# Optimization experiments

Measured on AMD Instinct MI355X. Metric: run time of the kernel, lower is better.

## Reference

```python
import jax, jax.numpy as jnp
import numpy as np
from math import sqrt

IN_DIM = 4096
OUT_DIM = 32
TW = 2            # tree_width (forced to 2 by the forward's pairwise stacking)
TREE_DEPTH = 22
T = TREE_DEPTH - 1  # number of loop iterations (module decrements tree_depth)


def _w(k, out_dim, in_dim):
    # mimics init_weights_unif: U(-1,1)/sqrt(out_dim) + eye (preserve=True default)
    x = (jax.random.uniform(k, (out_dim, in_dim)) * 2 - 1) / sqrt(out_dim)
    return x + jnp.eye(out_dim, in_dim)


def _b(k, dim):
    return (jax.random.uniform(k, (dim,)) * 2 - 1) / sqrt(dim)


def setup_inputs() -> dict:
    key = jax.random.key(0)
    ks = jax.random.split(key, 14)
    return {
        "x": jax.random.normal(ks[0], (IN_DIM,), dtype=jnp.float32),
        "in_left_layer": _w(ks[1], TW, IN_DIM),
        "in_right_layer": _w(ks[2], TW, IN_DIM),
        "in_left_bias": _b(ks[3], TW),
        "in_right_bias": _b(ks[4], TW),
        "tree_left_layers": jnp.stack([_w(k, TW, TW) for k in jax.random.split(ks[5], T)]),
        "tree_right_layers": jnp.stack([_w(k, TW, TW) for k in jax.random.split(ks[6], T)]),
        "tree_left_biases": jnp.stack([_b(k, TW) for k in jax.random.split(ks[7], T)]),
        "tree_right_biases": jnp.stack([_b(k, TW) for k in jax.random.split(ks[8], T)]),
        "out_layer0": _w(ks[9], OUT_DIM, IN_DIM),
        "out_layers": jnp.stack([_w(k, OUT_DIM, TW) for k in jax.random.split(ks[10], T)]),
        "out_bias": _b(ks[11], OUT_DIM),
    }


def reference(x, in_left_layer, in_right_layer, in_left_bias, in_right_bias,
              tree_left_layers, tree_right_layers, tree_left_biases,
              tree_right_biases, out_layer0, out_layers, out_bias):
    # Faithful to BinTreeNetwork.forward: the per-j torch.tensor([li_j, ri_j])
    # construction is exactly jnp.stack([left, right], axis=1); the
    # ComponentNetwork is constructed in __init__ but never used in forward.
    left = x @ in_left_layer.T + in_left_bias      # (TW,)
    right = x @ in_right_layer.T + in_right_bias   # (TW,)
    out = x @ out_layer0.T                          # (OUT_DIM,)
    n_iter = tree_left_layers.shape[0]
    for i in range(n_iter):  # fixed small structural loop; shapes differ per level
        # res: binary-tree expansion, shape (2,)*(i+2); res[j,0]=left[j], res[j,1]=right[j]
        res = jnp.stack([left, right], axis=1)
        left = res @ tree_left_layers[i].T + tree_left_biases[i]
        right = res @ tree_right_layers[i].T + tree_right_biases[i]
        # out broadcasts: (2,)*i+(OUT_DIM,) + (2,)*(i+1)+(OUT_DIM,)
        out = out + res @ out_layers[i].T
    return out + out_bias  # shape (2,)*T + (OUT_DIM,)
```

## Files before the change

kernel.cpp:

```cpp
#include <hip/hip_runtime.h>
#include <hip/hip_bf16.h>


#define P0 (1u << 19)
#define C14OFF (1u << 20)
#define C16OFF (1u << 21)

typedef float floatx4 __attribute__((ext_vector_type(4)));

__global__ __launch_bounds__(1024) void k_dots(
    const float* __restrict__ x,
    const float* __restrict__ inL,
    const float* __restrict__ inR,
    const float* __restrict__ outL0,
    float* __restrict__ ws)
{
    __shared__ float red[16];
    const int d = blockIdx.x;
    const int tid = threadIdx.x;
    const float* row =
        (d < 2) ? inL + d * 4096 :
        (d < 4) ? inR + (d - 2) * 4096 :
                  outL0 + (d - 4) * 4096;
    floatx4 a = ((const floatx4*)row)[tid];
    floatx4 b = ((const floatx4*)x)[tid];
    float s = a.x * b.x + a.y * b.y + a.z * b.z + a.w * b.w;
    #pragma unroll
    for (int off = 32; off; off >>= 1) s += __shfl_down(s, off, 64);
    if ((tid & 63) == 0) red[tid >> 6] = s;
    __syncthreads();
    if (tid < 16) {
        float v = red[tid];
        #pragma unroll
        for (int off = 8; off; off >>= 1) v += __shfl_down(v, off, 16);
        if (tid == 0) ws[P0 + 1664 + d] = v;
    }
}

__global__ __launch_bounds__(1024) void k_levels(
    const float* __restrict__ inLb,
    const float* __restrict__ inRb,
    const float* __restrict__ treeL,
    const float* __restrict__ treeR,
    const float* __restrict__ treeLb,
    const float* __restrict__ treeRb,
    const float* __restrict__ outLs,
    const float* __restrict__ outB,
    float* __restrict__ ws)
{
    const int tid = threadIdx.x;
    float* base  = ws + P0;
    float* outLf = ws + P0 + 32;
    float* tLf   = ws + P0 + 1376;
    float* tRf   = ws + P0 + 1460;
    float* tLbf  = ws + P0 + 1544;
    float* tRbf  = ws + P0 + 1586;
    const float* dots = ws + P0 + 1664;
    float* C7    = ws + P0 + 2048;

    for (int i = tid; i < 21 * 64; i += 1024) outLf[i] = outLs[i];
    if (tid < 84)                      tLf[tid]        = treeL[tid];
    else if (tid < 168)                tRf[tid - 84]   = treeR[tid - 84];
    else if (tid < 210)                tLbf[tid - 168] = treeLb[tid - 168];
    else if (tid < 252)                tRbf[tid - 210] = treeRb[tid - 210];
    if (tid < 32) base[tid] = dots[4 + tid] + outB[tid];
    if (tid < 2) {
        ws[tid * 2 + 0] = dots[tid]     + inLb[tid];
        ws[tid * 2 + 1] = dots[2 + tid] + inRb[tid];
    }
    __syncthreads();

    for (int i = 1; i <= 13; ++i) {
        const float* prev = ws + ((1u << (i + 1)) - 4);
        float* cur        = ws + ((1u << (i + 2)) - 4);
        const int rows = 1 << (i + 1);
        const int lowmask = (1 << (i - 1)) - 1;
        for (int m = tid; m < rows; m += 1024) {
            const int src = ((m >> i) << (i - 1)) | (m & lowmask);
            const int s = (m >> (i - 1)) & 1;
            const float* W  = (s ? tRf  : tLf)  + (i - 1) * 4;
            const float* bb = (s ? tRbf : tLbf) + (i - 1) * 2;
            const float p0 = prev[src * 2], p1 = prev[src * 2 + 1];
            cur[m * 2 + 0] = W[0] * p0 + W[1] * p1 + bb[0];
            cur[m * 2 + 1] = W[2] * p0 + W[3] * p1 + bb[1];
        }
        __syncthreads();
    }

    for (int idx = tid; idx < 8192; idx += 1024) {
        const int m = idx >> 5, o = idx & 31;
        float s = base[o];
        #pragma unroll
        for (int i = 0; i < 8; ++i) {
            const float* ri = ws + ((1u << (i + 2)) - 4) + (m & ((2 << i) - 1)) * 2;
            s += ri[0] * outLf[i * 64 + o * 2] + ri[1] * outLf[i * 64 + o * 2 + 1];
        }
        C7[idx] = s;
    }
}

__global__ __launch_bounds__(256) void k_mid(float* __restrict__ ws)
{
    const int blk = blockIdx.x;
    int j, b;
    if      (blk < 16) { j = 14; b = blk; }
    else if (blk < 48) { j = 15; b = blk - 16; }
    else               { j = 16; b = blk - 48; }

    const float* tLf  = ws + P0 + 1376;
    const float* tRf  = ws + P0 + 1460;
    const float* tLbf = ws + P0 + 1544;
    const float* tRbf = ws + P0 + 1586;

    unsigned m = (unsigned)b << 11;
    const unsigned basej = m;
    unsigned sbits = 0;
    for (int l = j; l > 13; --l) {
        sbits |= ((m >> (l - 1)) & 1u) << l;
        m = ((m >> l) << (l - 1)) | (m & ((1u << (l - 1)) - 1));
    }

    const int r0 = threadIdx.x * 8;
    const floatx4* s4 = (const floatx4*)(ws + ((1u << 15) - 4) + (m + r0) * 2);
    floatx4 a0 = s4[0], a1 = s4[1], a2 = s4[2], a3 = s4[3];
    float r[8][2] = {{a0.x,a0.y},{a0.z,a0.w},{a1.x,a1.y},{a1.z,a1.w},
                     {a2.x,a2.y},{a2.z,a2.w},{a3.x,a3.y},{a3.z,a3.w}};

    for (int l = 14; l <= j; ++l) {
        const int s = (sbits >> l) & 1;
        const float* W  = (s ? tRf  : tLf)  + (l - 1) * 4;
        const float* bb = (s ? tRbf : tLbf) + (l - 1) * 2;
        const float w00 = W[0], w01 = W[1], w10 = W[2], w11 = W[3];
        const float b0 = bb[0], b1 = bb[1];
        #pragma unroll
        for (int q = 0; q < 8; ++q) {
            const float p0 = r[q][0], p1 = r[q][1];
            r[q][0] = w00 * p0 + w01 * p1 + b0;
            r[q][1] = w10 * p0 + w11 * p1 + b1;
        }
    }

    floatx4* d4 = (floatx4*)(ws + ((1u << (j + 2)) - 4) + (basej + r0) * 2);
    d4[0] = (floatx4){r[0][0], r[0][1], r[1][0], r[1][1]};
    d4[1] = (floatx4){r[2][0], r[2][1], r[3][0], r[3][1]};
    d4[2] = (floatx4){r[4][0], r[4][1], r[5][0], r[5][1]};
    d4[3] = (floatx4){r[6][0], r[6][1], r[7][0], r[7][1]};
}

__global__ __launch_bounds__(256) void k_c16(float* __restrict__ ws)
{
    const unsigned m = blockIdx.x * 256u + threadIdx.x;
    const float* outLf = ws + P0 + 32;
    const float* C7    = ws + P0 + 2048;

    float acc[32];
    const floatx4* c4 = (const floatx4*)(C7 + (m & 255u) * 32);
    #pragma unroll
    for (int q = 0; q < 8; ++q) {
        floatx4 v = c4[q];
        acc[q * 4 + 0] = v.x; acc[q * 4 + 1] = v.y;
        acc[q * 4 + 2] = v.z; acc[q * 4 + 3] = v.w;
    }
    #pragma unroll
    for (int i = 8; i <= 16; ++i) {
        const float2 v = *(const float2*)(ws + ((1u << (i + 2)) - 4)
                                             + (m & ((2u << i) - 1)) * 2);
        const float* cf = outLf + i * 64;
        #pragma unroll
        for (int o = 0; o < 32; ++o)
            acc[o] += v.x * cf[o * 2] + v.y * cf[o * 2 + 1];
    }
    floatx4* dst = (floatx4*)(ws + C16OFF + (size_t)m * 32);
    #pragma unroll
    for (int q = 0; q < 8; ++q)
        dst[q] = (floatx4){acc[q * 4 + 0], acc[q * 4 + 1],
                           acc[q * 4 + 2], acc[q * 4 + 3]};
}

__global__ __launch_bounds__(256) void k_c14(float* __restrict__ ws)
{
    const unsigned m = blockIdx.x * 256u + threadIdx.x;
    const float* outLf = ws + P0 + 32;
    const float* C7    = ws + P0 + 2048;

    float acc[32];
    const floatx4* c4 = (const floatx4*)(C7 + (m & 255u) * 32);
    #pragma unroll
    for (int q = 0; q < 8; ++q) {
        floatx4 v = c4[q];
        acc[q * 4 + 0] = v.x; acc[q * 4 + 1] = v.y;
        acc[q * 4 + 2] = v.z; acc[q * 4 + 3] = v.w;
    }
    #pragma unroll
    for (int i = 8; i <= 14; ++i) {
        const float2 v = *(const float2*)(ws + ((1u << (i + 2)) - 4)
                                             + (m & ((2u << i) - 1)) * 2);
        const float* cf = outLf + i * 64;
        #pragma unroll
        for (int o = 0; o < 32; ++o)
            acc[o] += v.x * cf[o * 2] + v.y * cf[o * 2 + 1];
    }
    floatx4* dst = (floatx4*)(ws + C14OFF + m * 32);
    #pragma unroll
    for (int q = 0; q < 8; ++q)
        dst[q] = (floatx4){acc[q * 4 + 0], acc[q * 4 + 1],
                           acc[q * 4 + 2], acc[q * 4 + 3]};
}

__global__ __launch_bounds__(256) void k_final_c16(const float* __restrict__ ws,
                                                   float* __restrict__ out)
{
    __shared__ floatx4 st[256 * 8];
    const int tid = threadIdx.x;
    const unsigned B = blockIdx.x * 256u + tid;
    const float* outLf = ws + P0 + 32;
    const float* tLf   = ws + P0 + 1376;
    const float* tRf   = ws + P0 + 1460;
    const float* tLbf  = ws + P0 + 1544;
    const float* tRbf  = ws + P0 + 1586;
    const float* C16   = ws + C16OFF;

    float acc[32];
    {
        const floatx4* c4 = (const floatx4*)(C16 + (size_t)(B & 0x1FFFFu) * 32);
        #pragma unroll
        for (int q = 0; q < 8; ++q) {
            floatx4 v = c4[q];
            acc[q * 4 + 0] = v.x; acc[q * 4 + 1] = v.y;
            acc[q * 4 + 2] = v.z; acc[q * 4 + 3] = v.w;
        }
    }

    {
        const unsigned Blo = B & 0xFFFFu;
        const float* r16 = ws + ((1u << 18) - 4);
        float2 vA = *(const float2*)(r16 + Blo * 2);
        float2 vC = *(const float2*)(r16 + (Blo + 65536u) * 2);
        float A0 = vA.x, A1 = vA.y;
        float c0 = vC.x, c1 = vC.y;
        #pragma unroll
        for (int l = 17; l <= 20; ++l) {
            const int s = (B >> (l - 1)) & 1;
            const float* WL = tLf + (l - 1) * 4;
            const float* WR = tRf + (l - 1) * 4;
            const float* bL = tLbf + (l - 1) * 2;
            const float* bR = tRbf + (l - 1) * 2;
            const float w00 = s ? WR[0] : WL[0], w01 = s ? WR[1] : WL[1];
            const float w10 = s ? WR[2] : WL[2], w11 = s ? WR[3] : WL[3];
            const float b0  = s ? bR[0] : bL[0], b1  = s ? bR[1] : bL[1];
            const float nA0 = w00 * A0 + w01 * A1 + b0;
            const float nA1 = w10 * A0 + w11 * A1 + b1;
            const float nc0 = w00 * c0 + w01 * c1 + b0;
            const float nc1 = w10 * c0 + w11 * c1 + b1;
            A0 = nA0; A1 = nA1; c0 = nc0; c1 = nc1;
            const int pick = (B >> l) & 1;
            const float q0 = pick ? c0 : A0, q1 = pick ? c1 : A1;
            const float* cf = outLf + l * 64;
            #pragma unroll
            for (int o = 0; o < 32; ++o)
                acc[o] += q0 * cf[o * 2] + q1 * cf[o * 2 + 1];
        }
    }

    #pragma unroll
    for (int q = 0; q < 8; ++q) {
        st[tid * 8 + (q ^ (tid & 7))] =
            (floatx4){acc[q * 4 + 0], acc[q * 4 + 1],
                      acc[q * 4 + 2], acc[q * 4 + 3]};
    }
    __syncthreads();
    {
        const int w = tid >> 6, lane = tid & 63;
        const int x = (lane & 7) ^ (lane >> 3);
        floatx4* dst = (floatx4*)(out + (size_t)blockIdx.x * 8192u
                                      + (unsigned)w * 2048u + (unsigned)lane * 4u);
        #pragma unroll
        for (int j = 0; j < 8; ++j) {
            const int m = w * 64 + j * 8 + (lane >> 3);
            __builtin_nontemporal_store(st[m * 8 + x], dst + j * 64);
        }
    }
}

__global__ __launch_bounds__(256) void k_final_fold(const float* __restrict__ ws,
                                                    float* __restrict__ out)
{
    __shared__ floatx4 st[256 * 8];
    const int tid = threadIdx.x;
    const unsigned B = blockIdx.x * 256u + tid;
    const float* outLf = ws + P0 + 32;
    const float* tLf   = ws + P0 + 1376;
    const float* tRf   = ws + P0 + 1460;
    const float* tLbf  = ws + P0 + 1544;
    const float* tRbf  = ws + P0 + 1586;
    const float* C14   = ws + C14OFF;

    float acc[32];
    {
        const floatx4* c4 = (const floatx4*)(C14 + (B & 0x7FFFu) * 32);
        #pragma unroll
        for (int q = 0; q < 8; ++q) {
            floatx4 v = c4[q];
            acc[q * 4 + 0] = v.x; acc[q * 4 + 1] = v.y;
            acc[q * 4 + 2] = v.z; acc[q * 4 + 3] = v.w;
        }
    }
    {
        const float2 v = *(const float2*)(ws + ((1u << 17) - 4)
                                             + (B & 0xFFFFu) * 2);
        const float* cf = outLf + 15 * 64;
        #pragma unroll
        for (int o = 0; o < 32; ++o)
            acc[o] += v.x * cf[o * 2] + v.y * cf[o * 2 + 1];
    }
    {
        const unsigned Blo = B & 0xFFFFu;
        const float* r16 = ws + ((1u << 18) - 4);
        float2 vA = *(const float2*)(r16 + Blo * 2);
        float2 vC = *(const float2*)(r16 + (Blo + 65536u) * 2);
        float A0 = vA.x, A1 = vA.y;
        float c0 = vC.x, c1 = vC.y;
        {
            const int pick = (B >> 16) & 1;
            const float q0 = pick ? c0 : A0, q1 = pick ? c1 : A1;
            const float* cf = outLf + 16 * 64;
            #pragma unroll
            for (int o = 0; o < 32; ++o)
                acc[o] += q0 * cf[o * 2] + q1 * cf[o * 2 + 1];
        }
        #pragma unroll
        for (int l = 17; l <= 20; ++l) {
            const int s = (B >> (l - 1)) & 1;
            const float* WL = tLf + (l - 1) * 4;
            const float* WR = tRf + (l - 1) * 4;
            const float* bL = tLbf + (l - 1) * 2;
            const float* bR = tRbf + (l - 1) * 2;
            const float w00 = s ? WR[0] : WL[0], w01 = s ? WR[1] : WL[1];
            const float w10 = s ? WR[2] : WL[2], w11 = s ? WR[3] : WL[3];
            const float b0  = s ? bR[0] : bL[0], b1  = s ? bR[1] : bL[1];
            const float nA0 = w00 * A0 + w01 * A1 + b0;
            const float nA1 = w10 * A0 + w11 * A1 + b1;
            const float nc0 = w00 * c0 + w01 * c1 + b0;
            const float nc1 = w10 * c0 + w11 * c1 + b1;
            A0 = nA0; A1 = nA1; c0 = nc0; c1 = nc1;
            const int pick = (B >> l) & 1;
            const float q0 = pick ? c0 : A0, q1 = pick ? c1 : A1;
            const float* cf = outLf + l * 64;
            #pragma unroll
            for (int o = 0; o < 32; ++o)
                acc[o] += q0 * cf[o * 2] + q1 * cf[o * 2 + 1];
        }
    }
    #pragma unroll
    for (int q = 0; q < 8; ++q) {
        st[tid * 8 + (q ^ (tid & 7))] =
            (floatx4){acc[q * 4 + 0], acc[q * 4 + 1],
                      acc[q * 4 + 2], acc[q * 4 + 3]};
    }
    __syncthreads();
    {
        const int w = tid >> 6, lane = tid & 63;
        const int x = (lane & 7) ^ (lane >> 3);
        floatx4* dst = (floatx4*)(out + (size_t)blockIdx.x * 8192u
                                      + (unsigned)w * 2048u + (unsigned)lane * 4u);
        #pragma unroll
        for (int j = 0; j < 8; ++j) {
            const int m = w * 64 + j * 8 + (lane >> 3);
            __builtin_nontemporal_store(st[m * 8 + x], dst + j * 64);
        }
    }
}

__global__ __launch_bounds__(256) void k_final_legacy(const float* __restrict__ ws,
                                                      float* __restrict__ out)
{
    __shared__ floatx4 st[256 * 8];
    const int tid = threadIdx.x;
    const unsigned B = blockIdx.x * 256u + tid;
    const float* outLf = ws + P0 + 32;
    const float* tLf   = ws + P0 + 1376;
    const float* tRf   = ws + P0 + 1460;
    const float* tLbf  = ws + P0 + 1544;
    const float* tRbf  = ws + P0 + 1586;
    const float* C7    = ws + P0 + 2048;

    float acc[32];
    {
        const floatx4* c4 = (const floatx4*)(C7 + (B & 255u) * 32);
        #pragma unroll
        for (int q = 0; q < 8; ++q) {
            floatx4 v = c4[q];
            acc[q * 4 + 0] = v.x; acc[q * 4 + 1] = v.y;
            acc[q * 4 + 2] = v.z; acc[q * 4 + 3] = v.w;
        }
    }
    float p[8][2];
    #pragma unroll
    for (int i = 8; i <= 15; ++i) {
        const float2* ri = (const float2*)(ws + ((1u << (i + 2)) - 4)
                                              + (B & ((2u << i) - 1)) * 2);
        float2 v = *ri;
        p[i - 8][0] = v.x;
        p[i - 8][1] = v.y;
    }
    #pragma unroll
    for (int i = 0; i < 8; ++i) {
        const float* cf = outLf + (i + 8) * 64;
        const float q0 = p[i][0], q1 = p[i][1];
        #pragma unroll
        for (int o = 0; o < 32; ++o)
            acc[o] += q0 * cf[o * 2] + q1 * cf[o * 2 + 1];
    }
    {
        const unsigned Blo = B & 0xFFFFu;
        const float* r16 = ws + ((1u << 18) - 4);
        float2 vA = *(const float2*)(r16 + Blo * 2);
        float2 vC = *(const float2*)(r16 + (Blo + 65536u) * 2);
        float A0 = vA.x, A1 = vA.y;
        float c0 = vC.x, c1 = vC.y;
        {
            const int pick = (B >> 16) & 1;
            const float q0 = pick ? c0 : A0, q1 = pick ? c1 : A1;
            const float* cf = outLf + 16 * 64;
            #pragma unroll
            for (int o = 0; o < 32; ++o)
                acc[o] += q0 * cf[o * 2] + q1 * cf[o * 2 + 1];
        }
        #pragma unroll
        for (int l = 17; l <= 20; ++l) {
            const int s = (B >> (l - 1)) & 1;
            const float* WL = tLf + (l - 1) * 4;
            const float* WR = tRf + (l - 1) * 4;
            const float* bL = tLbf + (l - 1) * 2;
            const float* bR = tRbf + (l - 1) * 2;
            const float w00 = s ? WR[0] : WL[0], w01 = s ? WR[1] : WL[1];
            const float w10 = s ? WR[2] : WL[2], w11 = s ? WR[3] : WL[3];
            const float b0  = s ? bR[0] : bL[0], b1  = s ? bR[1] : bL[1];
            const float nA0 = w00 * A0 + w01 * A1 + b0;
            const float nA1 = w10 * A0 + w11 * A1 + b1;
            const float nc0 = w00 * c0 + w01 * c1 + b0;
            const float nc1 = w10 * c0 + w11 * c1 + b1;
            A0 = nA0; A1 = nA1; c0 = nc0; c1 = nc1;
            const int pick = (B >> l) & 1;
            const float q0 = pick ? c0 : A0, q1 = pick ? c1 : A1;
            const float* cf = outLf + l * 64;
            #pragma unroll
            for (int o = 0; o < 32; ++o)
                acc[o] += q0 * cf[o * 2] + q1 * cf[o * 2 + 1];
        }
    }
    #pragma unroll
    for (int q = 0; q < 8; ++q) {
        st[tid * 8 + (q ^ (tid & 7))] =
            (floatx4){acc[q * 4 + 0], acc[q * 4 + 1],
                      acc[q * 4 + 2], acc[q * 4 + 3]};
    }
    __syncthreads();
    {
        const int w = tid >> 6, lane = tid & 63;
        const int x = (lane & 7) ^ (lane >> 3);
        floatx4* dst = (floatx4*)(out + (size_t)blockIdx.x * 8192u
                                      + (unsigned)w * 2048u + (unsigned)lane * 4u);
        #pragma unroll
        for (int j = 0; j < 8; ++j) {
            const int m = w * 64 + j * 8 + (lane >> 3);
            __builtin_nontemporal_store(st[m * 8 + x], dst + j * 64);
        }
    }
}

extern "C" void kernel_launch(void* const* d_in, const int* in_sizes, int n_in,
                              void* d_out, int out_size, void* d_ws, size_t ws_size,
                              hipStream_t stream) {
    const float* x     = (const float*)d_in[0];
    const float* inL   = (const float*)d_in[1];
    const float* inR   = (const float*)d_in[2];
    const float* inLb  = (const float*)d_in[3];
    const float* inRb  = (const float*)d_in[4];
    const float* treeL = (const float*)d_in[5];
    const float* treeR = (const float*)d_in[6];
    const float* treeLb= (const float*)d_in[7];
    const float* treeRb= (const float*)d_in[8];
    const float* outL0 = (const float*)d_in[9];
    const float* outLs = (const float*)d_in[10];
    const float* outB  = (const float*)d_in[11];
    float* ws = (float*)d_ws;
    float* out = (float*)d_out;

    const bool use_c16 = ws_size >= ((size_t)C16OFF + (1u << 22)) * sizeof(float);
    const bool use_c14 = ws_size >= ((size_t)C14OFF + (1u << 20)) * sizeof(float);

    hipLaunchKernelGGL(k_dots, dim3(36), dim3(1024), 0, stream,
                       x, inL, inR, outL0, ws);
    hipLaunchKernelGGL(k_levels, dim3(1), dim3(1024), 0, stream,
                       inLb, inRb, treeL, treeR, treeLb, treeRb, outLs, outB, ws);
    hipLaunchKernelGGL(k_mid, dim3(112), dim3(256), 0, stream, ws);
    if (use_c16) {
        hipLaunchKernelGGL(k_c16, dim3(512), dim3(256), 0, stream, ws);
        hipLaunchKernelGGL(k_final_c16, dim3(1u << 13), dim3(256), 0, stream, ws, out);
    } else if (use_c14) {
        hipLaunchKernelGGL(k_c14, dim3(128), dim3(256), 0, stream, ws);
        hipLaunchKernelGGL(k_final_fold, dim3(1u << 13), dim3(256), 0, stream, ws, out);
    } else {
        hipLaunchKernelGGL(k_final_legacy, dim3(1u << 13), dim3(256), 0, stream, ws, out);
    }
}
```

Measured before the change: 360.4 us.

## Replace single-block level kernel with parallel per-node path recompute

On the large-workspace path, the single-block k_levels and k_mid kernels are replaced by k_paths. It launches one thread per tree node up to level 16, and each thread recomputes its node's value by walking the 2x2 affine chain from the root. k_c16f then builds the C16 table directly from all levels 0..16, and the final kernel reads weights straight from the inputs instead of workspace copies. The aim is to remove the serial one-block level stage and one launch. The cost is redundant per-thread chain work, up to 16 steps each.

```diff
diff --git a/kernel.cpp b/kernel.cpp
--- a/kernel.cpp
+++ b/kernel.cpp
@@ -34,6 +34,149 @@
         #pragma unroll
         for (int off = 8; off; off >>= 1) v += __shfl_down(v, off, 16);
         if (tid == 0) ws[P0 + 1664 + d] = v;
+    }
+}
+
+__global__ __launch_bounds__(256) void k_paths(
+    const float* __restrict__ treeL,
+    const float* __restrict__ treeR,
+    const float* __restrict__ treeLb,
+    const float* __restrict__ treeRb,
+    const float* __restrict__ inLb,
+    const float* __restrict__ inRb,
+    float* __restrict__ ws)
+{
+    const unsigned t = blockIdx.x * 256u + threadIdx.x;
+    const float* dots = ws + P0 + 1664;
+
+    if (t < 2) {
+        ws[t * 2 + 0] = dots[t]     + inLb[t];
+        ws[t * 2 + 1] = dots[2 + t] + inRb[t];
+    }
+    if (t >= (1u << 18) - 4) return;
+
+    const unsigned u = t + 4u;
+    const int i = (31 - __clz(u)) - 1;
+    unsigned m = u - (1u << (i + 1));
+    unsigned sbits = 0;
+    for (int l = i; l >= 1; --l) {
+        sbits |= ((m >> (l - 1)) & 1u) << l;
+        m = ((m >> l) << (l - 1)) | (m & ((1u << (l - 1)) - 1u));
+    }
+    float v0 = dots[m]     + inLb[m];
+    float v1 = dots[2 + m] + inRb[m];
+    for (int l = 1; l <= i; ++l) {
+        const int s = (sbits >> l) & 1;
+        const float* W  = (s ? treeR  : treeL)  + (l - 1) * 4;
+        const float* bb = (s ? treeRb : treeLb) + (l - 1) * 2;
+        const float n0 = W[0] * v0 + W[1] * v1 + bb[0];
+        const float n1 = W[2] * v0 + W[3] * v1 + bb[1];
+        v0 = n0; v1 = n1;
+    }
+    ws[2 * t + 4] = v0;
+    ws[2 * t + 5] = v1;
+}
+
+__global__ __launch_bounds__(256) void k_c16f(
+    const float* __restrict__ outLs,
+    const float* __restrict__ outB,
+    float* __restrict__ ws)
+{
+    const unsigned m = blockIdx.x * 256u + threadIdx.x;
+    const float* dots = ws + P0 + 1664;
+
+    float acc[32];
+    #pragma unroll
+    for (int o = 0; o < 32; ++o) acc[o] = dots[4 + o] + outB[o];
+    #pragma unroll
+    for (int i = 0; i <= 16; ++i) {
+        const float2 v = *(const float2*)(ws + ((1u << (i + 2)) - 4)
+                                             + (m & ((2u << i) - 1)) * 2);
+        const float* cf = outLs + i * 64;
+        #pragma unroll
+        for (int o = 0; o < 32; ++o)
+            acc[o] += v.x * cf[o * 2] + v.y * cf[o * 2 + 1];
+    }
+    floatx4* dst = (floatx4*)(ws + C16OFF + (size_t)m * 32);
+    #pragma unroll
+    for (int q = 0; q < 8; ++q)
+        dst[q] = (floatx4){acc[q * 4 + 0], acc[q * 4 + 1],
+                           acc[q * 4 + 2], acc[q * 4 + 3]};
+}
+
+__global__ __launch_bounds__(256) void k_final_c16(
+    const float* __restrict__ ws,
+    const float* __restrict__ outLs,
+    const float* __restrict__ treeL,
+    const float* __restrict__ treeR,
+    const float* __restrict__ treeLb,
+    const float* __restrict__ treeRb,
+    float* __restrict__ out)
+{
+    __shared__ floatx4 st[256 * 8];
+    const int tid = threadIdx.x;
+    const unsigned B = blockIdx.x * 256u + tid;
+    const float* C16 = ws + C16OFF;
+
+    float acc[32];
+    {
+        const floatx4* c4 = (const floatx4*)(C16 + (size_t)(B & 0x1FFFFu) * 32);
+        #pragma unroll
+        for (int q = 0; q < 8; ++q) {
+            floatx4 v = c4[q];
+            acc[q * 4 + 0] = v.x; acc[q * 4 + 1] = v.y;
+            acc[q * 4 + 2] = v.z; acc[q * 4 + 3] = v.w;
+        }
+    }
+
+    {
+        const unsigned Blo = B & 0xFFFFu;
+        const float* r16 = ws + ((1u << 18) - 4);
+        float2 vA = *(const float2*)(r16 + Blo * 2);
+        float2 vC = *(const float2*)(r16 + (Blo + 65536u) * 2);
+        float A0 = vA.x, A1 = vA.y;
+        float c0 = vC.x, c1 = vC.y;
+        #pragma unroll
+        for (int l = 17; l <= 20; ++l) {
+            const int s = (B >> (l - 1)) & 1;
+            const float* WL = treeL  + (l - 1) * 4;
+            const float* WR = treeR  + (l - 1) * 4;
+            const float* bL = treeLb + (l - 1) * 2;
+            const float* bR = treeRb + (l - 1) * 2;
+            const float w00 = s ? WR[0] : WL[0], w01 = s ? WR[1] : WL[1];
+            const float w10 = s ? WR[2] : WL[2], w11 = s ? WR[3] : WL[3];
+            const float b0  = s ? bR[0] : bL[0], b1  = s ? bR[1] : bL[1];
+            const float nA0 = w00 * A0 + w01 * A1 + b0;
+            const float nA1 = w10 * A0 + w11 * A1 + b1;
+            const float nc0 = w00 * c0 + w01 * c1 + b0;
+            const float nc1 = w10 * c0 + w11 * c1 + b1;
+            A0 = nA0; A1 = nA1; c0 = nc0; c1 = nc1;
+            const int pick = (B >> l) & 1;
+            const float q0 = pick ? c0 : A0, q1 = pick ? c1 : A1;
+            const float* cf = outLs + l * 64;
+            #pragma unroll
+            for (int o = 0; o < 32; ++o)
+                acc[o] += q0 * cf[o * 2] + q1 * cf[o * 2 + 1];
+        }
+    }
+
+    #pragma unroll
+    for (int q = 0; q < 8; ++q) {
+        st[tid * 8 + (q ^ (tid & 7))] =
+            (floatx4){acc[q * 4 + 0], acc[q * 4 + 1],
+                      acc[q * 4 + 2], acc[q * 4 + 3]};
+    }
+    __syncthreads();
+    {
+        const int w = tid >> 6, lane = tid & 63;
+        const int x = (lane & 7) ^ (lane >> 3);
+        floatx4* dst = (floatx4*)(out + (size_t)blockIdx.x * 8192u
+                                      + (unsigned)w * 2048u + (unsigned)lane * 4u);
+        #pragma unroll
+        for (int j = 0; j < 8; ++j) {
+            const int m = w * 64 + j * 8 + (lane >> 3);
+            __builtin_nontemporal_store(st[m * 8 + x], dst + j * 64);
+        }
     }
 }
 
@@ -147,7 +290,7 @@
     d4[3] = (floatx4){r[6][0], r[6][1], r[7][0], r[7][1]};
 }
 
-__global__ __launch_bounds__(256) void k_c16(float* __restrict__ ws)
+__global__ __launch_bounds__(256) void k_c14(float* __restrict__ ws)
 {
     const unsigned m = blockIdx.x * 256u + threadIdx.x;
     const float* outLf = ws + P0 + 32;
@@ -162,36 +305,6 @@
         acc[q * 4 + 2] = v.z; acc[q * 4 + 3] = v.w;
     }
     #pragma unroll
-    for (int i = 8; i <= 16; ++i) {
-        const float2 v = *(const float2*)(ws + ((1u << (i + 2)) - 4)
-                                             + (m & ((2u << i) - 1)) * 2);
-        const float* cf = outLf + i * 64;
-        #pragma unroll
-        for (int o = 0; o < 32; ++o)
-            acc[o] += v.x * cf[o * 2] + v.y * cf[o * 2 + 1];
-    }
-    floatx4* dst = (floatx4*)(ws + C16OFF + (size_t)m * 32);
-    #pragma unroll
-    for (int q = 0; q < 8; ++q)
-        dst[q] = (floatx4){acc[q * 4 + 0], acc[q * 4 + 1],
-                           acc[q * 4 + 2], acc[q * 4 + 3]};
-}
-
-__global__ __launch_bounds__(256) void k_c14(float* __restrict__ ws)
-{
-    const unsigned m = blockIdx.x * 256u + threadIdx.x;
-    const float* outLf = ws + P0 + 32;
-    const float* C7    = ws + P0 + 2048;
-
-    float acc[32];
-    const floatx4* c4 = (const floatx4*)(C7 + (m & 255u) * 32);
-    #pragma unroll
-    for (int q = 0; q < 8; ++q) {
-        floatx4 v = c4[q];
-        acc[q * 4 + 0] = v.x; acc[q * 4 + 1] = v.y;
-        acc[q * 4 + 2] = v.z; acc[q * 4 + 3] = v.w;
-    }
-    #pragma unroll
     for (int i = 8; i <= 14; ++i) {
         const float2 v = *(const float2*)(ws + ((1u << (i + 2)) - 4)
                                              + (m & ((2u << i) - 1)) * 2);
@@ -207,8 +320,8 @@
                            acc[q * 4 + 2], acc[q * 4 + 3]};
 }
 
-__global__ __launch_bounds__(256) void k_final_c16(const float* __restrict__ ws,
-                                                   float* __restrict__ out)
+__global__ __launch_bounds__(256) void k_final_fold(const float* __restrict__ ws,
+                                                    float* __restrict__ out)
 {
     __shared__ floatx4 st[256 * 8];
     const int tid = threadIdx.x;
@@ -218,11 +331,11 @@
     const float* tRf   = ws + P0 + 1460;
     const float* tLbf  = ws + P0 + 1544;
     const float* tRbf  = ws + P0 + 1586;
-    const float* C16   = ws + C16OFF;
+    const float* C14   = ws + C14OFF;
 
     float acc[32];
     {
-        const floatx4* c4 = (const floatx4*)(C16 + (size_t)(B & 0x1FFFFu) * 32);
+        const floatx4* c4 = (const floatx4*)(C14 + (B & 0x7FFFu) * 32);
         #pragma unroll
         for (int q = 0; q < 8; ++q) {
             floatx4 v = c4[q];
@@ -230,7 +343,14 @@
             acc[q * 4 + 2] = v.z; acc[q * 4 + 3] = v.w;
         }
     }
-
+    {
+        const float2 v = *(const float2*)(ws + ((1u << 17) - 4)
+                                             + (B & 0xFFFFu) * 2);
+        const float* cf = outLf + 15 * 64;
+        #pragma unroll
+        for (int o = 0; o < 32; ++o)
+            acc[o] += v.x * cf[o * 2] + v.y * cf[o * 2 + 1];
+    }
     {
         const unsigned Blo = B & 0xFFFFu;
         const float* r16 = ws + ((1u << 18) - 4);
@@ -238,6 +358,14 @@
         float2 vC = *(const float2*)(r16 + (Blo + 65536u) * 2);
         float A0 = vA.x, A1 = vA.y;
         float c0 = vC.x, c1 = vC.y;
+        {
+            const int pick = (B >> 16) & 1;
+            const float q0 = pick ? c0 : A0, q1 = pick ? c1 : A1;
+            const float* cf = outLf + 16 * 64;
+            #pragma unroll
+            for (int o = 0; o < 32; ++o)
+                acc[o] += q0 * cf[o * 2] + q1 * cf[o * 2 + 1];
+        }
         #pragma unroll
         for (int l = 17; l <= 20; ++l) {
             const int s = (B >> (l - 1)) & 1;
@@ -261,7 +389,6 @@
                 acc[o] += q0 * cf[o * 2] + q1 * cf[o * 2 + 1];
         }
     }
-
     #pragma unroll
     for (int q = 0; q < 8; ++q) {
         st[tid * 8 + (q ^ (tid & 7))] =
@@ -282,8 +409,8 @@
     }
 }
 
-__global__ __launch_bounds__(256) void k_final_fold(const float* __restrict__ ws,
-                                                    float* __restrict__ out)
+__global__ __launch_bounds__(256) void k_final_legacy(const float* __restrict__ ws,
+                                                      float* __restrict__ out)
 {
     __shared__ floatx4 st[256 * 8];
     const int tid = threadIdx.x;
@@ -293,11 +420,11 @@
     const float* tRf   = ws + P0 + 1460;
     const float* tLbf  = ws + P0 + 1544;
     const float* tRbf  = ws + P0 + 1586;
-    const float* C14   = ws + C14OFF;
+    const float* C7    = ws + P0 + 2048;
 
     float acc[32];
     {
-        const floatx4* c4 = (const floatx4*)(C14 + (B & 0x7FFFu) * 32);
+        const floatx4* c4 = (const floatx4*)(C7 + (B & 255u) * 32);
         #pragma unroll
         for (int q = 0; q < 8; ++q) {
             floatx4 v = c4[q];
@@ -305,13 +432,22 @@
             acc[q * 4 + 2] = v.z; acc[q * 4 + 3] = v.w;
         }
     }
-    {
-        const float2 v = *(const float2*)(ws + ((1u << 17) - 4)
-                                             + (B & 0xFFFFu) * 2);
-        const float* cf = outLf + 15 * 64;
+    float p[8][2];
+    #pragma unroll
+    for (int i = 8; i <= 15; ++i) {
+        const float2* ri = (const float2*)(ws + ((1u << (i + 2)) - 4)
+                                              + (B & ((2u << i) - 1)) * 2);
+        float2 v = *ri;
+        p[i - 8][0] = v.x;
+        p[i - 8][1] = v.y;
+    }
+    #pragma unroll
+    for (int i = 0; i < 8; ++i) {
+        const float* cf = outLf + (i + 8) * 64;
+        const float q0 = p[i][0], q1 = p[i][1];
         #pragma unroll
         for (int o = 0; o < 32; ++o)
-            acc[o] += v.x * cf[o * 2] + v.y * cf[o * 2 + 1];
+            acc[o] += q0 * cf[o * 2] + q1 * cf[o * 2 + 1];
     }
     {
         const unsigned Blo = B & 0xFFFFu;
@@ -371,104 +507,6 @@
     }
 }
 
-__global__ __launch_bounds__(256) void k_final_legacy(const float* __restrict__ ws,
-                                                      float* __restrict__ out)
-{
-    __shared__ floatx4 st[256 * 8];
-    const int tid = threadIdx.x;
-    const unsigned B = blockIdx.x * 256u + tid;
-    const float* outLf = ws + P0 + 32;
-    const float* tLf   = ws + P0 + 1376;
-    const float* tRf   = ws + P0 + 1460;
-    const float* tLbf  = ws + P0 + 1544;
-    const float* tRbf  = ws + P0 + 1586;
-    const float* C7    = ws + P0 + 2048;
-
-    float acc[32];
-    {
-        const floatx4* c4 = (const floatx4*)(C7 + (B & 255u) * 32);
-        #pragma unroll
-        for (int q = 0; q < 8; ++q) {
-            floatx4 v = c4[q];
-            acc[q * 4 + 0] = v.x; acc[q * 4 + 1] = v.y;
-            acc[q * 4 + 2] = v.z; acc[q * 4 + 3] = v.w;
-        }
-    }
-    float p[8][2];
-    #pragma unroll
-    for (int i = 8; i <= 15; ++i) {
-        const float2* ri = (const float2*)(ws + ((1u << (i + 2)) - 4)
-                                              + (B & ((2u << i) - 1)) * 2);
-        float2 v = *ri;
-        p[i - 8][0] = v.x;
-        p[i - 8][1] = v.y;
-    }
-    #pragma unroll
-    for (int i = 0; i < 8; ++i) {
-        const float* cf = outLf + (i + 8) * 64;
-        const float q0 = p[i][0], q1 = p[i][1];
-        #pragma unroll
-        for (int o = 0; o < 32; ++o)
-            acc[o] += q0 * cf[o * 2] + q1 * cf[o * 2 + 1];
-    }
-    {
-        const unsigned Blo = B & 0xFFFFu;
-        const float* r16 = ws + ((1u << 18) - 4);
-        float2 vA = *(const float2*)(r16 + Blo * 2);
-        float2 vC = *(const float2*)(r16 + (Blo + 65536u) * 2);
-        float A0 = vA.x, A1 = vA.y;
-        float c0 = vC.x, c1 = vC.y;
-        {
-            const int pick = (B >> 16) & 1;
-            const float q0 = pick ? c0 : A0, q1 = pick ? c1 : A1;
-            const float* cf = outLf + 16 * 64;
-            #pragma unroll
-            for (int o = 0; o < 32; ++o)
-                acc[o] += q0 * cf[o * 2] + q1 * cf[o * 2 + 1];
-        }
-        #pragma unroll
-        for (int l = 17; l <= 20; ++l) {
-            const int s = (B >> (l - 1)) & 1;
-            const float* WL = tLf + (l - 1) * 4;
-            const float* WR = tRf + (l - 1) * 4;
-            const float* bL = tLbf + (l - 1) * 2;
-            const float* bR = tRbf + (l - 1) * 2;
-            const float w00 = s ? WR[0] : WL[0], w01 = s ? WR[1] : WL[1];
-            const float w10 = s ? WR[2] : WL[2], w11 = s ? WR[3] : WL[3];
-            const float b0  = s ? bR[0] : bL[0], b1  = s ? bR[1] : bL[1];
-            const float nA0 = w00 * A0 + w01 * A1 + b0;
-            const float nA1 = w10 * A0 + w11 * A1 + b1;
-            const float nc0 = w00 * c0 + w01 * c1 + b0;
-            const float nc1 = w10 * c0 + w11 * c1 + b1;
-            A0 = nA0; A1 = nA1; c0 = nc0; c1 = nc1;
-            const int pick = (B >> l) & 1;
-            const float q0 = pick ? c0 : A0, q1 = pick ? c1 : A1;
-            const float* cf = outLf + l * 64;
-            #pragma unroll
-            for (int o = 0; o < 32; ++o)
-                acc[o] += q0 * cf[o * 2] + q1 * cf[o * 2 + 1];
-        }
-    }
-    #pragma unroll
-    for (int q = 0; q < 8; ++q) {
-        st[tid * 8 + (q ^ (tid & 7))] =
-            (floatx4){acc[q * 4 + 0], acc[q * 4 + 1],
-                      acc[q * 4 + 2], acc[q * 4 + 3]};
-    }
-    __syncthreads();
-    {
-        const int w = tid >> 6, lane = tid & 63;
-        const int x = (lane & 7) ^ (lane >> 3);
-        floatx4* dst = (floatx4*)(out + (size_t)blockIdx.x * 8192u
-                                      + (unsigned)w * 2048u + (unsigned)lane * 4u);
-        #pragma unroll
-        for (int j = 0; j < 8; ++j) {
-            const int m = w * 64 + j * 8 + (lane >> 3);
-            __builtin_nontemporal_store(st[m * 8 + x], dst + j * 64);
-        }
-    }
-}
-
 extern "C" void kernel_launch(void* const* d_in, const int* in_sizes, int n_in,
                               void* d_out, int out_size, void* d_ws, size_t ws_size,
                               hipStream_t stream) {
@@ -492,16 +530,22 @@
 
     hipLaunchKernelGGL(k_dots, dim3(36), dim3(1024), 0, stream,
                        x, inL, inR, outL0, ws);
-    hipLaunchKernelGGL(k_levels, dim3(1), dim3(1024), 0, stream,
-                       inLb, inRb, treeL, treeR, treeLb, treeRb, outLs, outB, ws);
-    hipLaunchKernelGGL(k_mid, dim3(112), dim3(256), 0, stream, ws);
     if (use_c16) {
-        hipLaunchKernelGGL(k_c16, dim3(512), dim3(256), 0, stream, ws);
-        hipLaunchKernelGGL(k_final_c16, dim3(1u << 13), dim3(256), 0, stream, ws, out);
-    } else if (use_c14) {
-        hipLaunchKernelGGL(k_c14, dim3(128), dim3(256), 0, stream, ws);
-        hipLaunchKernelGGL(k_final_fold, dim3(1u << 13), dim3(256), 0, stream, ws, out);
+        hipLaunchKernelGGL(k_paths, dim3(1024), dim3(256), 0, stream,
+                           treeL, treeR, treeLb, treeRb, inLb, inRb, ws);
+        hipLaunchKernelGGL(k_c16f, dim3(512), dim3(256), 0, stream,
+                           outLs, outB, ws);
+        hipLaunchKernelGGL(k_final_c16, dim3(1u << 13), dim3(256), 0, stream,
+                           ws, outLs, treeL, treeR, treeLb, treeRb, out);
     } else {
-        hipLaunchKernelGGL(k_final_legacy, dim3(1u << 13), dim3(256), 0, stream, ws, out);
-    }
-}
+        hipLaunchKernelGGL(k_levels, dim3(1), dim3(1024), 0, stream,
+                           inLb, inRb, treeL, treeR, treeLb, treeRb, outLs, outB, ws);
+        hipLaunchKernelGGL(k_mid, dim3(112), dim3(256), 0, stream, ws);
+        if (use_c14) {
+            hipLaunchKernelGGL(k_c14, dim3(128), dim3(256), 0, stream, ws);
+            hipLaunchKernelGGL(k_final_fold, dim3(1u << 13), dim3(256), 0, stream, ws, out);
+        } else {
+            hipLaunchKernelGGL(k_final_legacy, dim3(1u << 13), dim3(256), 0, stream, ws, out);
+        }
+    }
+}
```

Result: faster. 334.7 us (-7.1%).
